# Kernel optimization log

Hardware: AMD Instinct MI355X
Metric: run time of the kernel (lower is better)

The kernel has to match this reference:

```python
import jax, jax.numpy as jnp
import numpy as np

PI_2 = 3.14159 / 2  # matches the torch module's pi_2 constant
EPS = 1e-8          # F.cosine_similarity default eps


def setup_inputs() -> dict:
    key = jax.random.key(0)
    k1, k2 = jax.random.split(key)
    B, N, C, H, W = 32, 2000, 512, 7, 7
    key_t = jax.random.normal(k1, (B, C, H, W), dtype=jnp.float32)
    memory = jax.random.normal(k2, (N, C, H, W), dtype=jnp.float32)
    return {"key": key_t, "memory": memory}


def reference(key, memory):
    # Memory.read(key): cosine-similarity addressing + tan warp + softmax, then weighted read.
    B = key.shape[0]
    N = memory.shape[0]
    k = key.reshape(B, -1)        # [B, D], D = C*H*W
    m = memory.reshape(N, -1)     # [N, D]
    # cosine similarity with torch's eps clamping on norms
    dots = jnp.einsum('bd,nd->bn', k, m)                                   # [B, N]
    k_norm = jnp.maximum(jnp.sqrt(jnp.sum(k * k, axis=-1, keepdims=True)), EPS)  # [B, 1]
    m_norm = jnp.maximum(jnp.sqrt(jnp.sum(m * m, axis=-1)), EPS)                 # [N]
    cos = dots / (k_norm * m_norm[None, :])                                 # [B, N]
    w = jax.nn.softmax(jnp.tan(cos * PI_2), axis=1)                         # [B, N]
    # weighted read: sum_n w[b,n] * memory[n,c,h,w] -> [B, C, H, W]
    out = jnp.einsum('bn,nchw->bchw', w, memory)
    return out
```

## Files before the change

kernel.cpp:

```cpp
#include <hip/hip_runtime.h>
#include <math.h>

#define D_ELEMS 25088
#define D4      6272
#define N_MEM   2000
#define B_KEYS  32
#define PI_2F   1.570795f
#define EPSF    1e-8f
#define NSLICE  16
#define KSLICE  1568
#define KSTEPS  49

using short8 = __attribute__((ext_vector_type(8))) short;
using short4v = __attribute__((ext_vector_type(4))) short;
using f32x4  = __attribute__((ext_vector_type(4))) float;


__device__ inline short f2bf(float x) {
    union { float f; unsigned u; } v; v.f = x;
    unsigned r = v.u + 0x7fffu + ((v.u >> 16) & 1u);
    return (short)(r >> 16);
}

__global__ __launch_bounds__(256) void k_prep(const float* __restrict__ key,
                                              short* __restrict__ keyb) {
    const int i = blockIdx.x * 256 + threadIdx.x;
    const float4 f = ((const float4*)key)[i];
    short4v s; s[0] = f2bf(f.x); s[1] = f2bf(f.y); s[2] = f2bf(f.z); s[3] = f2bf(f.w);
    ((short4v*)keyb)[i] = s;
}

__global__ __launch_bounds__(64) void k_dots_mfma(const short* __restrict__ keyb,
                                                  const float* __restrict__ mem,
                                                  float* __restrict__ dots_part,
                                                  float* __restrict__ mn2_part) {
    const int nt   = blockIdx.x / NSLICE;
    const int s    = blockIdx.x % NSLICE;
    const int n0   = nt * 16;
    const int lane = threadIdx.x;
    const int quad = lane >> 4;
    const int l16  = lane & 15;
    const int k0   = s * KSLICE + quad * 8;

    const short* a0p = keyb + (size_t)l16 * D_ELEMS + k0;
    const short* a1p = keyb + (size_t)(16 + l16) * D_ELEMS + k0;
    const float4* bp = (const float4*)(mem + (size_t)(n0 + l16) * D_ELEMS + k0);

    f32x4 acc0 = {0.f, 0.f, 0.f, 0.f};
    f32x4 acc1 = {0.f, 0.f, 0.f, 0.f};
    float msq = 0.f;

    short8 a0 = *(const short8*)a0p;
    short8 a1 = *(const short8*)a1p;
    float4 f0 = bp[0], f1 = bp[1];

    for (int t = 0; t < KSTEPS; ++t) {
        const short8 a0c = a0, a1c = a1;
        const float4 f0c = f0, f1c = f1;
        if (t + 1 < KSTEPS) {
            a0 = *(const short8*)(a0p + (t + 1) * 32);
            a1 = *(const short8*)(a1p + (t + 1) * 32);
            f0 = bp[(t + 1) * 8];
            f1 = bp[(t + 1) * 8 + 1];
        }
        msq += f0c.x * f0c.x + f0c.y * f0c.y + f0c.z * f0c.z + f0c.w * f0c.w
             + f1c.x * f1c.x + f1c.y * f1c.y + f1c.z * f1c.z + f1c.w * f1c.w;
        short8 b;
        b[0] = f2bf(f0c.x); b[1] = f2bf(f0c.y); b[2] = f2bf(f0c.z); b[3] = f2bf(f0c.w);
        b[4] = f2bf(f1c.x); b[5] = f2bf(f1c.y); b[6] = f2bf(f1c.z); b[7] = f2bf(f1c.w);
        acc0 = __builtin_amdgcn_mfma_f32_16x16x32_bf16(a0c, b, acc0, 0, 0, 0);
        acc1 = __builtin_amdgcn_mfma_f32_16x16x32_bf16(a1c, b, acc1, 0, 0, 0);
    }

    float* dp = dots_part + (size_t)(s * N_MEM + n0 + l16) * B_KEYS;
#pragma unroll
    for (int r = 0; r < 4; ++r) {
        dp[quad * 4 + r]      = acc0[r];
        dp[16 + quad * 4 + r] = acc1[r];
    }

    msq += __shfl_xor(msq, 16, 64);
    msq += __shfl_xor(msq, 32, 64);
    if (lane < 16) mn2_part[s * N_MEM + n0 + lane] = msq;
}

__global__ __launch_bounds__(256) void k_reduce(const float* __restrict__ dots_part,
                                                const float* __restrict__ mn2_part,
                                                float* __restrict__ dots,
                                                float* __restrict__ mn2) {
    const int gid = blockIdx.x * 256 + threadIdx.x;
    float ds = 0.f;
#pragma unroll
    for (int s = 0; s < NSLICE; ++s) ds += dots_part[s * (N_MEM * B_KEYS) + gid];
    dots[gid] = ds;
    if (gid < N_MEM) {
        float ms = 0.f;
#pragma unroll
        for (int s = 0; s < NSLICE; ++s) ms += mn2_part[s * N_MEM + gid];
        mn2[gid] = ms;
    }
}

__global__ __launch_bounds__(512) void k_softmax(const float* __restrict__ key,
                                                 const float* __restrict__ dots,
                                                 const float* __restrict__ mn2,
                                                 float* __restrict__ w) {
    const int b   = blockIdx.x;
    const int tid = threadIdx.x;
    __shared__ float sred[512];
    __shared__ float xbuf[N_MEM];

    const float4* K4 = (const float4*)(key + (size_t)b * D_ELEMS);
    float ks = 0.f;
    for (int i = tid; i < D4; i += 512) {
        float4 kf = K4[i];
        ks += kf.x * kf.x + kf.y * kf.y + kf.z * kf.z + kf.w * kf.w;
    }
    sred[tid] = ks;
    __syncthreads();
    for (int o = 256; o; o >>= 1) {
        if (tid < o) sred[tid] += sred[tid + o];
        __syncthreads();
    }
    const float knorm = fmaxf(sqrtf(sred[0]), EPSF);
    __syncthreads();

    float mx = -1e30f;
    for (int n = tid; n < N_MEM; n += 512) {
        float mn = fmaxf(sqrtf(mn2[n]), EPSF);
        float x  = __tanf((dots[n * B_KEYS + b] / (knorm * mn)) * PI_2F);
        xbuf[n] = x;
        mx = fmaxf(mx, x);
    }
    sred[tid] = mx;
    __syncthreads();
    for (int o = 256; o; o >>= 1) {
        if (tid < o) sred[tid] = fmaxf(sred[tid], sred[tid + o]);
        __syncthreads();
    }
    mx = sred[0];
    __syncthreads();

    float sm = 0.f;
    for (int n = tid; n < N_MEM; n += 512) sm += __expf(xbuf[n] - mx);
    sred[tid] = sm;
    __syncthreads();
    for (int o = 256; o; o >>= 1) {
        if (tid < o) sred[tid] += sred[tid + o];
        __syncthreads();
    }
    const float inv = 1.f / sred[0];
    __syncthreads();

    for (int n = tid; n < N_MEM; n += 512)
        w[n * B_KEYS + b] = __expf(xbuf[n] - mx) * inv;
}

__global__ __launch_bounds__(256, 3) void k_read(const float* __restrict__ mem,
                                                 const float* __restrict__ w,
                                                 float* __restrict__ partial,
                                                 int nPerS) {
    const int db   = blockIdx.x % 98;
    const int s    = blockIdx.x / 98;
    const int n0   = s * nPerS;
    const int bg   = threadIdx.x >> 6;
    const int lane = threadIdx.x & 63;
    const int d4   = db * 64 + lane;

    const float4* M4 = (const float4*)mem;
    const float4* W4 = (const float4*)w;
    __shared__ float4 wls4[250 * 8];

    float acc[8][4];
#pragma unroll
    for (int i = 0; i < 8; ++i)
#pragma unroll
        for (int j = 0; j < 4; ++j) acc[i][j] = 0.f;

    for (int c0 = 0; c0 < nPerS; c0 += 250) {
        const int cn = 250;
        __syncthreads();
        for (int i = threadIdx.x; i < cn * 8; i += 256)
            wls4[i] = W4[(n0 + c0) * 8 + i];
        __syncthreads();

        const float4* mp = M4 + (size_t)(n0 + c0) * D4 + d4;
        float4 mv0 = mp[0];
        float4 mv1 = mp[(size_t)D4];
        for (int nn = 0; nn < cn; nn += 2) {
            const float4 mc0 = mv0;
            const int i2 = (nn + 2 < cn) ? nn + 2 : cn - 2;
            mv0 = mp[(size_t)i2 * D4];
            {
                const float4 wa = wls4[nn * 8 + bg * 2];
                const float4 wb = wls4[nn * 8 + bg * 2 + 1];
                const float wv[8] = {wa.x, wa.y, wa.z, wa.w, wb.x, wb.y, wb.z, wb.w};
#pragma unroll
                for (int i = 0; i < 8; ++i) {
                    acc[i][0] += wv[i] * mc0.x;
                    acc[i][1] += wv[i] * mc0.y;
                    acc[i][2] += wv[i] * mc0.z;
                    acc[i][3] += wv[i] * mc0.w;
                }
            }
            const float4 mc1 = mv1;
            const int i3 = (nn + 3 < cn) ? nn + 3 : cn - 1;
            mv1 = mp[(size_t)i3 * D4];
            {
                const float4 wa = wls4[(nn + 1) * 8 + bg * 2];
                const float4 wb = wls4[(nn + 1) * 8 + bg * 2 + 1];
                const float wv[8] = {wa.x, wa.y, wa.z, wa.w, wb.x, wb.y, wb.z, wb.w};
#pragma unroll
                for (int i = 0; i < 8; ++i) {
                    acc[i][0] += wv[i] * mc1.x;
                    acc[i][1] += wv[i] * mc1.y;
                    acc[i][2] += wv[i] * mc1.z;
                    acc[i][3] += wv[i] * mc1.w;
                }
            }
        }
    }

    float4* P4 = (float4*)partial;
#pragma unroll
    for (int i = 0; i < 8; ++i)
        P4[(size_t)(s * B_KEYS + bg * 8 + i) * D4 + d4] =
            make_float4(acc[i][0], acc[i][1], acc[i][2], acc[i][3]);
}

__global__ __launch_bounds__(256) void k_finish(const float* __restrict__ partial,
                                                float* __restrict__ out, int ns) {
    const int i = blockIdx.x * 256 + threadIdx.x;
    const float4* P4 = (const float4*)partial;
    float4 sum = P4[i];
    for (int s = 1; s < ns; ++s) {
        const float4 p = P4[(size_t)s * (B_KEYS * D4) + i];
        sum.x += p.x; sum.y += p.y; sum.z += p.z; sum.w += p.w;
    }
    ((float4*)out)[i] = sum;
}

extern "C" void kernel_launch(void* const* d_in, const int* in_sizes, int n_in,
                              void* d_out, int out_size, void* d_ws, size_t ws_size,
                              hipStream_t stream) {
    (void)in_sizes; (void)n_in; (void)out_size;
    const float* key = (const float*)d_in[0];
    const float* mem = (const float*)d_in[1];
    float* out = (float*)d_out;
    float* ws  = (float*)d_ws;

    short* keyb      = (short*)ws;
    float* dots_part = ws + 401408;
    float* mn2_part  = ws + 1425408;
    float* dots      = ws + 1457408;
    float* mn2       = ws + 1521408;
    float* w         = ws + 1523456;
    float* part      = ws + 1587456;

    int ns = 8;
    while (ns > 1 && (size_t)(1587456 + (size_t)ns * 802816) * 4 > ws_size) ns >>= 1;
    const int nPerS = N_MEM / ns;

    k_prep     <<<784, 256, 0, stream>>>(key, keyb);
    k_dots_mfma<<<125 * NSLICE, 64, 0, stream>>>(keyb, mem, dots_part, mn2_part);
    k_reduce   <<<250, 256, 0, stream>>>(dots_part, mn2_part, dots, mn2);
    k_softmax  <<<B_KEYS, 512, 0, stream>>>(key, dots, mn2, w);
    k_read     <<<98 * ns, 256, 0, stream>>>(mem, w, part, nPerS);
    k_finish   <<<784, 256, 0, stream>>>(part, out, ns);
}
```

Before: 396.6 us.

## Replace split-K partial buffers with atomic accumulation and fuse key norm into prep

The dots kernel now uses 49 K-slices and atomically adds its results into zeroed dots/mn2 buffers, which removes the separate reduce kernel. The read kernel splits N into 10 chunks of 200 and atomically adds into the output, which removes the partial buffer and the finish kernel. Key norms are computed during bf16 conversion instead of re-reading the key in softmax, and softmax caches exp values. The read kernel's loads are prefetched five deep and its occupancy hint is raised to 4. In exchange it adds a zeroing kernel, heavy float atomic traffic (about 8M atomics on the output), and a summation order that is no longer deterministic.

```diff
diff --git a/kernel.cpp b/kernel.cpp
--- a/kernel.cpp
+++ b/kernel.cpp
@@ -7,9 +7,11 @@
 #define B_KEYS  32
 #define PI_2F   1.570795f
 #define EPSF    1e-8f
-#define NSLICE  16
-#define KSLICE  1568
-#define KSTEPS  49
+#define NSLICE  49
+#define KSLICE  512
+#define KSTEPS  16
+#define NSPLIT  10
+#define NPS     200
 
 using short8 = __attribute__((ext_vector_type(8))) short;
 using short4v = __attribute__((ext_vector_type(4))) short;
@@ -22,18 +24,44 @@
     return (short)(r >> 16);
 }
 
+__global__ __launch_bounds__(256) void k_zero(float* __restrict__ out,
+                                              float* __restrict__ dots,
+                                              float* __restrict__ mn2) {
+    const int i = blockIdx.x * 256 + threadIdx.x;
+    const float4 z = make_float4(0.f, 0.f, 0.f, 0.f);
+    ((float4*)out)[i] = z;
+    if (i < 16000) ((float4*)dots)[i] = z;
+    if (i < 500)   ((float4*)mn2)[i] = z;
+}
+
 __global__ __launch_bounds__(256) void k_prep(const float* __restrict__ key,
-                                              short* __restrict__ keyb) {
-    const int i = blockIdx.x * 256 + threadIdx.x;
-    const float4 f = ((const float4*)key)[i];
-    short4v s; s[0] = f2bf(f.x); s[1] = f2bf(f.y); s[2] = f2bf(f.z); s[3] = f2bf(f.w);
-    ((short4v*)keyb)[i] = s;
+                                              short* __restrict__ keyb,
+                                              float* __restrict__ knorm) {
+    const int b   = blockIdx.x;
+    const int tid = threadIdx.x;
+    const float4* K4 = (const float4*)(key + (size_t)b * D_ELEMS);
+    short4v* KB4 = (short4v*)keyb + (size_t)b * D4;
+    float ks = 0.f;
+    for (int i = tid; i < D4; i += 256) {
+        const float4 f = K4[i];
+        short4v s;
+        s[0] = f2bf(f.x); s[1] = f2bf(f.y); s[2] = f2bf(f.z); s[3] = f2bf(f.w);
+        KB4[i] = s;
+        ks += f.x * f.x + f.y * f.y + f.z * f.z + f.w * f.w;
+    }
+#pragma unroll
+    for (int o = 1; o < 64; o <<= 1) ks += __shfl_xor(ks, o, 64);
+    __shared__ float sred[4];
+    if ((tid & 63) == 0) sred[tid >> 6] = ks;
+    __syncthreads();
+    if (tid == 0)
+        knorm[b] = fmaxf(sqrtf(sred[0] + sred[1] + sred[2] + sred[3]), EPSF);
 }
 
 __global__ __launch_bounds__(64) void k_dots_mfma(const short* __restrict__ keyb,
                                                   const float* __restrict__ mem,
-                                                  float* __restrict__ dots_part,
-                                                  float* __restrict__ mn2_part) {
+                                                  float* __restrict__ dots,
+                                                  float* __restrict__ mn2) {
     const int nt   = blockIdx.x / NSLICE;
     const int s    = blockIdx.x % NSLICE;
     const int n0   = nt * 16;
@@ -72,36 +100,19 @@
         acc1 = __builtin_amdgcn_mfma_f32_16x16x32_bf16(a1c, b, acc1, 0, 0, 0);
     }
 
-    float* dp = dots_part + (size_t)(s * N_MEM + n0 + l16) * B_KEYS;
+    float* dp = dots + (size_t)(n0 + l16) * B_KEYS;
 #pragma unroll
     for (int r = 0; r < 4; ++r) {
-        dp[quad * 4 + r]      = acc0[r];
-        dp[16 + quad * 4 + r] = acc1[r];
+        atomicAdd(dp + quad * 4 + r,      acc0[r]);
+        atomicAdd(dp + 16 + quad * 4 + r, acc1[r]);
     }
 
     msq += __shfl_xor(msq, 16, 64);
     msq += __shfl_xor(msq, 32, 64);
-    if (lane < 16) mn2_part[s * N_MEM + n0 + lane] = msq;
-}
-
-__global__ __launch_bounds__(256) void k_reduce(const float* __restrict__ dots_part,
-                                                const float* __restrict__ mn2_part,
-                                                float* __restrict__ dots,
-                                                float* __restrict__ mn2) {
-    const int gid = blockIdx.x * 256 + threadIdx.x;
-    float ds = 0.f;
-#pragma unroll
-    for (int s = 0; s < NSLICE; ++s) ds += dots_part[s * (N_MEM * B_KEYS) + gid];
-    dots[gid] = ds;
-    if (gid < N_MEM) {
-        float ms = 0.f;
-#pragma unroll
-        for (int s = 0; s < NSLICE; ++s) ms += mn2_part[s * N_MEM + gid];
-        mn2[gid] = ms;
-    }
-}
-
-__global__ __launch_bounds__(512) void k_softmax(const float* __restrict__ key,
+    if (lane < 16) atomicAdd(&mn2[n0 + lane], msq);
+}
+
+__global__ __launch_bounds__(512) void k_softmax(const float* __restrict__ knormArr,
                                                  const float* __restrict__ dots,
                                                  const float* __restrict__ mn2,
                                                  float* __restrict__ w) {
@@ -109,67 +120,55 @@
     const int tid = threadIdx.x;
     __shared__ float sred[512];
     __shared__ float xbuf[N_MEM];
-
-    const float4* K4 = (const float4*)(key + (size_t)b * D_ELEMS);
-    float ks = 0.f;
-    for (int i = tid; i < D4; i += 512) {
-        float4 kf = K4[i];
-        ks += kf.x * kf.x + kf.y * kf.y + kf.z * kf.z + kf.w * kf.w;
-    }
-    sred[tid] = ks;
+    const float knorm = knormArr[b];
+
+    float mx = -1e30f;
+    for (int n = tid; n < N_MEM; n += 512) {
+        const float mn = fmaxf(sqrtf(mn2[n]), EPSF);
+        const float x  = __tanf((dots[n * B_KEYS + b] / (knorm * mn)) * PI_2F);
+        xbuf[n] = x;
+        mx = fmaxf(mx, x);
+    }
+    sred[tid] = mx;
+    __syncthreads();
+    for (int o = 256; o; o >>= 1) {
+        if (tid < o) sred[tid] = fmaxf(sred[tid], sred[tid + o]);
+        __syncthreads();
+    }
+    mx = sred[0];
+    __syncthreads();
+
+    float sm = 0.f;
+    for (int n = tid; n < N_MEM; n += 512) {
+        const float e = __expf(xbuf[n] - mx);
+        xbuf[n] = e;
+        sm += e;
+    }
+    sred[tid] = sm;
     __syncthreads();
     for (int o = 256; o; o >>= 1) {
         if (tid < o) sred[tid] += sred[tid + o];
         __syncthreads();
     }
-    const float knorm = fmaxf(sqrtf(sred[0]), EPSF);
-    __syncthreads();
-
-    float mx = -1e30f;
-    for (int n = tid; n < N_MEM; n += 512) {
-        float mn = fmaxf(sqrtf(mn2[n]), EPSF);
-        float x  = __tanf((dots[n * B_KEYS + b] / (knorm * mn)) * PI_2F);
-        xbuf[n] = x;
-        mx = fmaxf(mx, x);
-    }
-    sred[tid] = mx;
-    __syncthreads();
-    for (int o = 256; o; o >>= 1) {
-        if (tid < o) sred[tid] = fmaxf(sred[tid], sred[tid + o]);
-        __syncthreads();
-    }
-    mx = sred[0];
-    __syncthreads();
-
-    float sm = 0.f;
-    for (int n = tid; n < N_MEM; n += 512) sm += __expf(xbuf[n] - mx);
-    sred[tid] = sm;
-    __syncthreads();
-    for (int o = 256; o; o >>= 1) {
-        if (tid < o) sred[tid] += sred[tid + o];
-        __syncthreads();
-    }
     const float inv = 1.f / sred[0];
-    __syncthreads();
 
     for (int n = tid; n < N_MEM; n += 512)
-        w[n * B_KEYS + b] = __expf(xbuf[n] - mx) * inv;
-}
-
-__global__ __launch_bounds__(256, 3) void k_read(const float* __restrict__ mem,
+        w[n * B_KEYS + b] = xbuf[n] * inv;
+}
+
+__global__ __launch_bounds__(256, 4) void k_read(const float* __restrict__ mem,
                                                  const float* __restrict__ w,
-                                                 float* __restrict__ partial,
-                                                 int nPerS) {
+                                                 float* __restrict__ out) {
     const int db   = blockIdx.x % 98;
     const int s    = blockIdx.x / 98;
-    const int n0   = s * nPerS;
+    const int n0   = s * NPS;
     const int bg   = threadIdx.x >> 6;
     const int lane = threadIdx.x & 63;
     const int d4   = db * 64 + lane;
 
     const float4* M4 = (const float4*)mem;
     const float4* W4 = (const float4*)w;
-    __shared__ float4 wls4[250 * 8];
+    __shared__ float4 wls4[NPS * 8];
 
     float acc[8][4];
 #pragma unroll
@@ -177,94 +176,69 @@
 #pragma unroll
         for (int j = 0; j < 4; ++j) acc[i][j] = 0.f;
 
-    for (int c0 = 0; c0 < nPerS; c0 += 250) {
-        const int cn = 250;
-        __syncthreads();
-        for (int i = threadIdx.x; i < cn * 8; i += 256)
-            wls4[i] = W4[(n0 + c0) * 8 + i];
-        __syncthreads();
-
-        const float4* mp = M4 + (size_t)(n0 + c0) * D4 + d4;
-        float4 mv0 = mp[0];
-        float4 mv1 = mp[(size_t)D4];
-        for (int nn = 0; nn < cn; nn += 2) {
-            const float4 mc0 = mv0;
-            const int i2 = (nn + 2 < cn) ? nn + 2 : cn - 2;
-            mv0 = mp[(size_t)i2 * D4];
-            {
-                const float4 wa = wls4[nn * 8 + bg * 2];
-                const float4 wb = wls4[nn * 8 + bg * 2 + 1];
-                const float wv[8] = {wa.x, wa.y, wa.z, wa.w, wb.x, wb.y, wb.z, wb.w};
-#pragma unroll
-                for (int i = 0; i < 8; ++i) {
-                    acc[i][0] += wv[i] * mc0.x;
-                    acc[i][1] += wv[i] * mc0.y;
-                    acc[i][2] += wv[i] * mc0.z;
-                    acc[i][3] += wv[i] * mc0.w;
-                }
-            }
-            const float4 mc1 = mv1;
-            const int i3 = (nn + 3 < cn) ? nn + 3 : cn - 1;
-            mv1 = mp[(size_t)i3 * D4];
-            {
-                const float4 wa = wls4[(nn + 1) * 8 + bg * 2];
-                const float4 wb = wls4[(nn + 1) * 8 + bg * 2 + 1];
-                const float wv[8] = {wa.x, wa.y, wa.z, wa.w, wb.x, wb.y, wb.z, wb.w};
-#pragma unroll
-                for (int i = 0; i < 8; ++i) {
-                    acc[i][0] += wv[i] * mc1.x;
-                    acc[i][1] += wv[i] * mc1.y;
-                    acc[i][2] += wv[i] * mc1.z;
-                    acc[i][3] += wv[i] * mc1.w;
-                }
-            }
-        }
-    }
-
-    float4* P4 = (float4*)partial;
-#pragma unroll
-    for (int i = 0; i < 8; ++i)
-        P4[(size_t)(s * B_KEYS + bg * 8 + i) * D4 + d4] =
-            make_float4(acc[i][0], acc[i][1], acc[i][2], acc[i][3]);
-}
-
-__global__ __launch_bounds__(256) void k_finish(const float* __restrict__ partial,
-                                                float* __restrict__ out, int ns) {
-    const int i = blockIdx.x * 256 + threadIdx.x;
-    const float4* P4 = (const float4*)partial;
-    float4 sum = P4[i];
-    for (int s = 1; s < ns; ++s) {
-        const float4 p = P4[(size_t)s * (B_KEYS * D4) + i];
-        sum.x += p.x; sum.y += p.y; sum.z += p.z; sum.w += p.w;
-    }
-    ((float4*)out)[i] = sum;
+    for (int i = threadIdx.x; i < NPS * 8; i += 256)
+        wls4[i] = W4[(size_t)n0 * 8 + i];
+    __syncthreads();
+
+    const float4* mp = M4 + (size_t)n0 * D4 + d4;
+    float4 mv0 = mp[0];
+    float4 mv1 = mp[(size_t)1 * D4];
+    float4 mv2 = mp[(size_t)2 * D4];
+    float4 mv3 = mp[(size_t)3 * D4];
+    float4 mv4 = mp[(size_t)4 * D4];
+
+#define RD_FMA(K, MV)                                                         \
+    {                                                                         \
+        const float4 mc = MV;                                                 \
+        const int ip = nn + 5 + (K);                                          \
+        MV = mp[(size_t)(ip < NPS ? ip : NPS - 1) * D4];                      \
+        const float4 wa = wls4[(nn + (K)) * 8 + bg * 2];                      \
+        const float4 wb = wls4[(nn + (K)) * 8 + bg * 2 + 1];                  \
+        const float wv[8] = {wa.x, wa.y, wa.z, wa.w, wb.x, wb.y, wb.z, wb.w}; \
+        _Pragma("unroll")                                                     \
+        for (int i = 0; i < 8; ++i) {                                         \
+            acc[i][0] += wv[i] * mc.x;                                        \
+            acc[i][1] += wv[i] * mc.y;                                        \
+            acc[i][2] += wv[i] * mc.z;                                        \
+            acc[i][3] += wv[i] * mc.w;                                        \
+        }                                                                     \
+    }
+
+    for (int nn = 0; nn < NPS; nn += 5) {
+        RD_FMA(0, mv0)
+        RD_FMA(1, mv1)
+        RD_FMA(2, mv2)
+        RD_FMA(3, mv3)
+        RD_FMA(4, mv4)
+    }
+#undef RD_FMA
+
+#pragma unroll
+    for (int i = 0; i < 8; ++i) {
+        float* op = out + (size_t)(bg * 8 + i) * D_ELEMS + (size_t)d4 * 4;
+#pragma unroll
+        for (int j = 0; j < 4; ++j) atomicAdd(op + j, acc[i][j]);
+    }
 }
 
 extern "C" void kernel_launch(void* const* d_in, const int* in_sizes, int n_in,
                               void* d_out, int out_size, void* d_ws, size_t ws_size,
                               hipStream_t stream) {
-    (void)in_sizes; (void)n_in; (void)out_size;
+    (void)in_sizes; (void)n_in; (void)out_size; (void)ws_size;
     const float* key = (const float*)d_in[0];
     const float* mem = (const float*)d_in[1];
     float* out = (float*)d_out;
     float* ws  = (float*)d_ws;
 
-    short* keyb      = (short*)ws;
-    float* dots_part = ws + 401408;
-    float* mn2_part  = ws + 1425408;
-    float* dots      = ws + 1457408;
-    float* mn2       = ws + 1521408;
-    float* w         = ws + 1523456;
-    float* part      = ws + 1587456;
-
-    int ns = 8;
-    while (ns > 1 && (size_t)(1587456 + (size_t)ns * 802816) * 4 > ws_size) ns >>= 1;
-    const int nPerS = N_MEM / ns;
-
-    k_prep     <<<784, 256, 0, stream>>>(key, keyb);
-    k_dots_mfma<<<125 * NSLICE, 64, 0, stream>>>(keyb, mem, dots_part, mn2_part);
-    k_reduce   <<<250, 256, 0, stream>>>(dots_part, mn2_part, dots, mn2);
-    k_softmax  <<<B_KEYS, 512, 0, stream>>>(key, dots, mn2, w);
-    k_read     <<<98 * ns, 256, 0, stream>>>(mem, w, part, nPerS);
-    k_finish   <<<784, 256, 0, stream>>>(part, out, ns);
-}
+    short* keyb  = (short*)ws;
+    float* dots  = ws + 401408;
+    float* mn2   = ws + 465408;
+    float* knorm = ws + 467408;
+    float* w     = ws + 467440;
+
+    k_zero     <<<784, 256, 0, stream>>>(out, dots, mn2);
+    k_prep     <<<B_KEYS, 256, 0, stream>>>(key, keyb, knorm);
+    k_dots_mfma<<<125 * NSLICE, 64, 0, stream>>>(keyb, mem, dots, mn2);
+    k_softmax  <<<B_KEYS, 512, 0, stream>>>(knorm, dots, mn2, w);
+    k_read     <<<98 * NSPLIT, 256, 0, stream>>>(mem, w, out);
+}
```

Measured after the change: 544.1 us. 1.37x slower.
